# Performance work log

Measured on AMD Instinct MI355X. Metric: run time of the kernel, lower is better.

The kernel has to match this reference:

```python
import jax, jax.numpy as jnp
import numpy as np

# ---- static config (mirrors build() with the chosen init_kwargs) ----
B, H, W, C = 16, 56, 56, 128
KH, KW = 3, 3          # filter_size
SH, SW = 1, 1          # stride
NF = 256               # n_filters
IN_FEAT = C * KH * KW  # 1152
NNZ = int(1 * 0.2 * IN_FEAT * NF)  # multiple * density * n_parameters = 58982


def _make_indices():
    """Replicates the full='output' sparsity-pattern construction from build()."""
    rng = np.random.default_rng(0)
    per_col = NNZ // NF
    remain = NNZ % NF
    remain_cols = set(rng.choice(NF, remain, replace=False).tolist())
    chunks = []
    for col in rng.permutation(NF):
        k = per_col + (1 if int(col) in remain_cols else 0)
        rows = rng.choice(IN_FEAT, k, replace=False)
        chunks.append(np.stack([rows, np.full(k, col, dtype=np.int64)], axis=1))
    return np.concatenate(chunks, axis=0).astype(np.int32)  # (NNZ, 2) [row, col]


def setup_inputs() -> dict:
    key = jax.random.key(0)
    k1, k2 = jax.random.split(key)
    x = jax.random.normal(k1, (B, H, W, C), dtype=jnp.float32)
    limit = float(np.sqrt(6.0 / (IN_FEAT + NF)))  # glorot_uniform on the sparse values
    kernel = jax.random.uniform(k2, (NNZ,), jnp.float32, -limit, limit)
    bias = jnp.zeros((NF,), jnp.float32)
    indices = jnp.asarray(_make_indices())
    return {"x": x, "kernel": kernel, "bias": bias, "indices": indices}


def _im2col_valid(x):
    # tf.image.extract_patches ordering: patch positions row-major (di, dj),
    # channels fastest -> concatenate C-channel slices in (di, dj) order.
    oh = (H - KH) // SH + 1
    ow = (W - KW) // SW + 1
    cols = [x[:, di:di + oh * SH:SH, dj:dj + ow * SW:SW, :]
            for di in range(KH) for dj in range(KW)]
    return jnp.concatenate(cols, axis=-1), oh, ow  # (B, oh, ow, IN_FEAT)


def reference(x, kernel, bias, indices):
    patches, oh, ow = _im2col_valid(x)
    pm = patches.reshape(-1, IN_FEAT)  # (B*oh*ow, IN_FEAT)
    # Sparse (IN_FEAT, NF) weight: scatter values into a dense matrix
    # (indices are unique by construction, so .add == .set and is grad-safe).
    Wm = jnp.zeros((IN_FEAT, NF), dtype=pm.dtype).at[indices[:, 0], indices[:, 1]].add(kernel)
    out = pm @ Wm + bias            # sparse-dense matmul + bias
    out = jax.nn.relu(out)          # activation
    return out.reshape(B, oh, ow, NF)
```

## Files before the change

### kernel.cpp

```cpp
#include <hip/hip_runtime.h>

typedef unsigned short u16;
typedef __bf16 bf16x8 __attribute__((ext_vector_type(8)));
typedef float f32x16 __attribute__((ext_vector_type(16)));

#define B_   16
#define H_   56
#define W_   56
#define C_   128
#define OH_  54
#define OW_  54
#define NF_  256
#define KF_  1152
#define M_   46656
#define NNZ_ 58982

#define XB_ELEMS (B_*H_*W_*C_)
#define WT_ELEMS (36*4*256*8)

__device__ __forceinline__ u16 f2bf(float f) {
    unsigned u = __float_as_uint(f);
    u += 0x7FFFu + ((u >> 16) & 1u);
    return (u16)(u >> 16);
}

__device__ __forceinline__ void gload16(const void* g, void* l) {
    __builtin_amdgcn_global_load_lds(
        (const __attribute__((address_space(1))) unsigned int*)g,
        (__attribute__((address_space(3))) unsigned int*)l,
        16, 0, 0);
}

__global__ __launch_bounds__(256) void cvt_x_kernel(const float* __restrict__ x,
                                                    u16* __restrict__ xb,
                                                    u16* __restrict__ wt) {
    if (blockIdx.x < 144) {
        uint4 z = {0u, 0u, 0u, 0u};
        ((uint4*)wt)[blockIdx.x * 256 + threadIdx.x] = z;
    }
    int i = (blockIdx.x * 256 + threadIdx.x) * 8;
    float4 v0 = *(const float4*)(x + i);
    float4 v1 = *(const float4*)(x + i + 4);
    union { u16 u[8]; uint4 v; } r;
    r.u[0] = f2bf(v0.x); r.u[1] = f2bf(v0.y); r.u[2] = f2bf(v0.z); r.u[3] = f2bf(v0.w);
    r.u[4] = f2bf(v1.x); r.u[5] = f2bf(v1.y); r.u[6] = f2bf(v1.z); r.u[7] = f2bf(v1.w);
    *(uint4*)(xb + i) = r.v;
}

__global__ __launch_bounds__(256) void scatter_kernel(const float* __restrict__ kv,
                                                      const int* __restrict__ idx,
                                                      u16* __restrict__ wt) {
    int t = blockIdx.x * 256 + threadIdx.x;
    if (t >= NNZ_) return;
    int k   = idx[2*t];
    int col = idx[2*t + 1];
    int kt = k >> 5, ks = (k >> 3) & 3, e = k & 7;
    wt[(kt * 4 + ks) * 2048 + col * 8 + e] = f2bf(kv[t]);
}

__global__ __launch_bounds__(128, 2) void spconv_gemm(const u16* __restrict__ xb,
                                                      const u16* __restrict__ wt,
                                                      const float* __restrict__ bias,
                                                      float* __restrict__ out) {
    __shared__ __align__(16) u16 As[2][64 * 32];

    const int t   = threadIdx.x;
    const int l   = t & 63;
    const int w   = t >> 6;
    const int l31 = l & 31;
    const int hi  = l >> 5;

    const int nwg = gridDim.x;
    const int q = nwg >> 3, r = nwg & 7;
    const int xcd = blockIdx.x & 7, inner = blockIdx.x >> 3;
    const int wg = (xcd < r ? xcd * (q + 1) : r * (q + 1) + (xcd - r) * q) + inner;
    const int m0 = wg * 64;

    const int row0 = t >> 2;
    const int kco  = ((t & 3) ^ ((t >> 2) & 3)) * 8;
    const u16* a_base0;
    const u16* a_base1;
    {
#define MKBASE(dst, mg) do {                                   \
        int bb_  = (mg) / (OH_ * OW_);                         \
        int rem_ = (mg) % (OH_ * OW_);                         \
        int ii_  = rem_ / OW_;                                 \
        int jj_  = rem_ % OW_;                                 \
        dst = xb + ((bb_ * H_ + ii_) * W_ + jj_) * C_;         \
    } while (0)
        MKBASE(a_base0, m0 + row0);
        MKBASE(a_base1, m0 + row0 + 32);
#undef MKBASE
    }

    const char* wtb = (const char*)wt;
    const char* b0 = wtb + hi * 4096 + w * 2048 + l31 * 16;
    const char* b1 = b0 + 8192;

    int aoffr[2][2];
#pragma unroll
    for (int rb = 0; rb < 2; ++rb)
#pragma unroll
        for (int kp = 0; kp < 2; ++kp)
            aoffr[rb][kp] = ((rb * 32 + l31) * 4 + ((kp * 2 + hi) ^ (l & 3))) * 8;

    f32x16 acc[2][4];
#pragma unroll
    for (int i = 0; i < 2; ++i)
#pragma unroll
        for (int j = 0; j < 4; ++j) acc[i][j] = (f32x16)0.f;

    bf16x8 bS0[8], bS1[8];

#define LOADB(dst, base, imm) \
    asm volatile("global_load_dwordx4 %0, %1, off offset:" imm \
                 : "=v"(dst) : "v"(base) : "memory")

#define ISSUE_A(kn, bi) do {                                                \
    int g_  = (kn) >> 2;                                                    \
    int di_ = (g_ * 11) >> 5;                                               \
    int dj_ = g_ - 3 * di_;                                                 \
    int aoff_ = (di_ * W_ + dj_) * C_ + ((kn) & 3) * 32 + kco;              \
    gload16(a_base0 + aoff_, &As[bi][t * 8]);                               \
    gload16(a_base1 + aoff_, &As[bi][(t + 128) * 8]);                       \
} while (0)

#define ISSUE_B(bset) do {                                                  \
    LOADB(bset[0], b0, "0");    LOADB(bset[1], b0, "512");                  \
    LOADB(bset[2], b0, "1024"); LOADB(bset[3], b0, "1536");                 \
    LOADB(bset[4], b1, "0");    LOADB(bset[5], b1, "512");                  \
    LOADB(bset[6], b1, "1024"); LOADB(bset[7], b1, "1536");                 \
    b0 += 16384; b1 += 16384;                                               \
} while (0)

#define COMPUTE(bi, bset) do {                                              \
    bf16x8 af_[2][2];                                                       \
    _Pragma("unroll")                                                       \
    for (int rb = 0; rb < 2; ++rb)                                          \
        _Pragma("unroll")                                                   \
        for (int kp = 0; kp < 2; ++kp)                                      \
            af_[rb][kp] = *(const bf16x8*)(&As[bi][aoffr[rb][kp]]);         \
    _Pragma("unroll")                                                       \
    for (int kp = 0; kp < 2; ++kp)                                          \
        _Pragma("unroll")                                                   \
        for (int rb = 0; rb < 2; ++rb)                                      \
            _Pragma("unroll")                                               \
            for (int cb = 0; cb < 4; ++cb)                                  \
                acc[rb][cb] = __builtin_amdgcn_mfma_f32_32x32x16_bf16(      \
                    af_[rb][kp], bset[kp * 4 + cb], acc[rb][cb], 0, 0, 0);  \
} while (0)

#define WAITVM(n) asm volatile("s_waitcnt vmcnt(" #n ")" ::: "memory")
#define WAITLG0() asm volatile("s_waitcnt lgkmcnt(0)" ::: "memory")
#define SB0()     __builtin_amdgcn_sched_barrier(0)
#define BAR() do { __builtin_amdgcn_s_barrier();                            \
                   asm volatile("" ::: "memory"); } while (0)

    ISSUE_A(0, 0); ISSUE_B(bS0);
    ISSUE_A(1, 1); ISSUE_B(bS1);

    for (int k2 = 0; k2 < 17; ++k2) {
        int kn0 = 2 * k2 + 2, kn1 = 2 * k2 + 3;
        WAITVM(10); SB0(); BAR();
        COMPUTE(0, bS0);
        WAITLG0(); BAR();
        ISSUE_A(kn0, 0); ISSUE_B(bS0);
        WAITVM(10); SB0(); BAR();
        COMPUTE(1, bS1);
        WAITLG0(); BAR();
        ISSUE_A(kn1, 1); ISSUE_B(bS1);
    }
    WAITVM(10); SB0(); BAR(); COMPUTE(0, bS0);
    WAITVM(0);  SB0(); BAR(); COMPUTE(1, bS1);

#undef LOADB
#undef ISSUE_A
#undef ISSUE_B
#undef COMPUTE
#undef WAITVM
#undef WAITLG0
#undef SB0
#undef BAR

#pragma unroll
    for (int cb = 0; cb < 4; ++cb) {
        int col  = w * 128 + cb * 32 + l31;
        float bv = bias[col];
#pragma unroll
        for (int rb = 0; rb < 2; ++rb) {
#pragma unroll
            for (int rg = 0; rg < 16; ++rg) {
                int row = m0 + rb * 32 + (rg & 3) + 8 * (rg >> 2) + 4 * hi;
                out[row * NF_ + col] = fmaxf(acc[rb][cb][rg] + bv, 0.f);
            }
        }
    }
}

extern "C" void kernel_launch(void* const* d_in, const int* in_sizes, int n_in,
                              void* d_out, int out_size, void* d_ws, size_t ws_size,
                              hipStream_t stream) {
    const float* x    = (const float*)d_in[0];
    const float* kv   = (const float*)d_in[1];
    const float* bias = (const float*)d_in[2];
    const int*   idx  = (const int*)d_in[3];
    float* out = (float*)d_out;

    u16* xb  = (u16*)d_ws;
    u16* wtp = (u16*)((char*)d_ws + (size_t)XB_ELEMS * 2);

    cvt_x_kernel<<<XB_ELEMS / (256 * 8), 256, 0, stream>>>(x, xb, wtp);
    scatter_kernel<<<(NNZ_ + 255) / 256, 256, 0, stream>>>(kv, idx, wtp);
    spconv_gemm<<<M_ / 64, 128, 0, stream>>>(xb, wtp, bias, out);
}
```

Measured before the change: 45.66 us.

## Split GEMM tile across eight waves with smaller per-wave sub-tiles

The 64x256 output tile per workgroup is now computed by 8 waves (2 row groups x 4 column groups) instead of 2, so each wave holds a 32x64 accumulator and loads a quarter of the B fragments. Only half the threads issue the A-tile loads into LDS, the wait counts are adjusted per thread group, and the LDS swizzle is changed to spread bank accesses. The aim is higher occupancy and more latency hiding through lower per-wave register pressure. In exchange, each wave does less MFMA work per LDS/global load and every workgroup hits more barriers.

```diff
diff --git a/kernel.cpp b/kernel.cpp
--- a/kernel.cpp
+++ b/kernel.cpp
@@ -58,7 +58,7 @@
     wt[(kt * 4 + ks) * 2048 + col * 8 + e] = f2bf(kv[t]);
 }
 
-__global__ __launch_bounds__(128, 2) void spconv_gemm(const u16* __restrict__ xb,
+__global__ __launch_bounds__(512, 4) void spconv_gemm(const u16* __restrict__ xb,
                                                       const u16* __restrict__ wt,
                                                       const float* __restrict__ bias,
                                                       float* __restrict__ out) {
@@ -69,6 +69,8 @@
     const int w   = t >> 6;
     const int l31 = l & 31;
     const int hi  = l >> 5;
+    const int wr  = w >> 2;
+    const int wc  = w & 3;
 
     const int nwg = gridDim.x;
     const int q = nwg >> 3, r = nwg & 7;
@@ -76,102 +78,84 @@
     const int wg = (xcd < r ? xcd * (q + 1) : r * (q + 1) + (xcd - r) * q) + inner;
     const int m0 = wg * 64;
 
-    const int row0 = t >> 2;
-    const int kco  = ((t & 3) ^ ((t >> 2) & 3)) * 8;
-    const u16* a_base0;
-    const u16* a_base1;
+    const int arow = (t & 255) >> 2;
+    const int kco  = (((t & 3) ^ (arow & 3) ^ ((arow >> 2) & 3))) * 8;
+    const u16* a_base;
     {
-#define MKBASE(dst, mg) do {                                   \
-        int bb_  = (mg) / (OH_ * OW_);                         \
-        int rem_ = (mg) % (OH_ * OW_);                         \
-        int ii_  = rem_ / OW_;                                 \
-        int jj_  = rem_ % OW_;                                 \
-        dst = xb + ((bb_ * H_ + ii_) * W_ + jj_) * C_;         \
-    } while (0)
-        MKBASE(a_base0, m0 + row0);
-        MKBASE(a_base1, m0 + row0 + 32);
-#undef MKBASE
+        int mg  = m0 + arow;
+        int bb  = mg / (OH_ * OW_);
+        int rem = mg % (OH_ * OW_);
+        int ii  = rem / OW_;
+        int jj  = rem % OW_;
+        a_base = xb + ((bb * H_ + ii) * W_ + jj) * C_;
     }
 
+    const int fr = (l31 & 3) ^ ((l31 >> 2) & 3);
+    int aoff0 = (wr * 32 + l31) * 32 + ((0 * 2 + hi) ^ fr) * 8;
+    int aoff1 = (wr * 32 + l31) * 32 + ((1 * 2 + hi) ^ fr) * 8;
+
     const char* wtb = (const char*)wt;
-    const char* b0 = wtb + hi * 4096 + w * 2048 + l31 * 16;
+    const char* b0 = wtb + hi * 4096 + (wc * 64 + l31) * 16;
     const char* b1 = b0 + 8192;
 
-    int aoffr[2][2];
-#pragma unroll
-    for (int rb = 0; rb < 2; ++rb)
-#pragma unroll
-        for (int kp = 0; kp < 2; ++kp)
-            aoffr[rb][kp] = ((rb * 32 + l31) * 4 + ((kp * 2 + hi) ^ (l & 3))) * 8;
+    f32x16 acc[2];
+    acc[0] = (f32x16)0.f; acc[1] = (f32x16)0.f;
 
-    f32x16 acc[2][4];
-#pragma unroll
-    for (int i = 0; i < 2; ++i)
-#pragma unroll
-        for (int j = 0; j < 4; ++j) acc[i][j] = (f32x16)0.f;
-
-    bf16x8 bS0[8], bS1[8];
+    bf16x8 bS0[4], bS1[4];
 
 #define LOADB(dst, base, imm) \
     asm volatile("global_load_dwordx4 %0, %1, off offset:" imm \
                  : "=v"(dst) : "v"(base) : "memory")
 
 #define ISSUE_A(kn, bi) do {                                                \
-    int g_  = (kn) >> 2;                                                    \
-    int di_ = (g_ * 11) >> 5;                                               \
-    int dj_ = g_ - 3 * di_;                                                 \
-    int aoff_ = (di_ * W_ + dj_) * C_ + ((kn) & 3) * 32 + kco;              \
-    gload16(a_base0 + aoff_, &As[bi][t * 8]);                               \
-    gload16(a_base1 + aoff_, &As[bi][(t + 128) * 8]);                       \
+    if (t < 256) {                                                          \
+        int g_  = (kn) >> 2;                                                \
+        int di_ = (g_ * 11) >> 5;                                           \
+        int dj_ = g_ - 3 * di_;                                             \
+        int aoff_ = (di_ * W_ + dj_) * C_ + ((kn) & 3) * 32 + kco;          \
+        gload16(a_base + aoff_, &As[bi][t * 8]);                            \
+    }                                                                       \
 } while (0)
 
 #define ISSUE_B(bset) do {                                                  \
-    LOADB(bset[0], b0, "0");    LOADB(bset[1], b0, "512");                  \
-    LOADB(bset[2], b0, "1024"); LOADB(bset[3], b0, "1536");                 \
-    LOADB(bset[4], b1, "0");    LOADB(bset[5], b1, "512");                  \
-    LOADB(bset[6], b1, "1024"); LOADB(bset[7], b1, "1536");                 \
+    LOADB(bset[0], b0, "0");   LOADB(bset[1], b0, "512");                   \
+    LOADB(bset[2], b1, "0");   LOADB(bset[3], b1, "512");                   \
     b0 += 16384; b1 += 16384;                                               \
 } while (0)
 
 #define COMPUTE(bi, bset) do {                                              \
-    bf16x8 af_[2][2];                                                       \
-    _Pragma("unroll")                                                       \
-    for (int rb = 0; rb < 2; ++rb)                                          \
-        _Pragma("unroll")                                                   \
-        for (int kp = 0; kp < 2; ++kp)                                      \
-            af_[rb][kp] = *(const bf16x8*)(&As[bi][aoffr[rb][kp]]);         \
-    _Pragma("unroll")                                                       \
-    for (int kp = 0; kp < 2; ++kp)                                          \
-        _Pragma("unroll")                                                   \
-        for (int rb = 0; rb < 2; ++rb)                                      \
-            _Pragma("unroll")                                               \
-            for (int cb = 0; cb < 4; ++cb)                                  \
-                acc[rb][cb] = __builtin_amdgcn_mfma_f32_32x32x16_bf16(      \
-                    af_[rb][kp], bset[kp * 4 + cb], acc[rb][cb], 0, 0, 0);  \
+    bf16x8 af0_ = *(const bf16x8*)(&As[bi][aoff0]);                         \
+    acc[0] = __builtin_amdgcn_mfma_f32_32x32x16_bf16(af0_, bset[0], acc[0], 0, 0, 0); \
+    acc[1] = __builtin_amdgcn_mfma_f32_32x32x16_bf16(af0_, bset[1], acc[1], 0, 0, 0); \
+    bf16x8 af1_ = *(const bf16x8*)(&As[bi][aoff1]);                         \
+    acc[0] = __builtin_amdgcn_mfma_f32_32x32x16_bf16(af1_, bset[2], acc[0], 0, 0, 0); \
+    acc[1] = __builtin_amdgcn_mfma_f32_32x32x16_bf16(af1_, bset[3], acc[1], 0, 0, 0); \
 } while (0)
 
-#define WAITVM(n) asm volatile("s_waitcnt vmcnt(" #n ")" ::: "memory")
+#define WAITVM(nb, na) do {                                                 \
+    if (t < 256) { asm volatile("s_waitcnt vmcnt(" #nb ")" ::: "memory"); } \
+    else         { asm volatile("s_waitcnt vmcnt(" #na ")" ::: "memory"); } \
+} while (0)
 #define WAITLG0() asm volatile("s_waitcnt lgkmcnt(0)" ::: "memory")
-#define SB0()     __builtin_amdgcn_sched_barrier(0)
 #define BAR() do { __builtin_amdgcn_s_barrier();                            \
                    asm volatile("" ::: "memory"); } while (0)
 
     ISSUE_A(0, 0); ISSUE_B(bS0);
     ISSUE_A(1, 1); ISSUE_B(bS1);
 
+#pragma unroll
     for (int k2 = 0; k2 < 17; ++k2) {
-        int kn0 = 2 * k2 + 2, kn1 = 2 * k2 + 3;
-        WAITVM(10); SB0(); BAR();
+        WAITVM(5, 4); BAR();
         COMPUTE(0, bS0);
         WAITLG0(); BAR();
-        ISSUE_A(kn0, 0); ISSUE_B(bS0);
-        WAITVM(10); SB0(); BAR();
+        ISSUE_A(2 * k2 + 2, 0); ISSUE_B(bS0);
+        WAITVM(5, 4); BAR();
         COMPUTE(1, bS1);
         WAITLG0(); BAR();
-        ISSUE_A(kn1, 1); ISSUE_B(bS1);
+        ISSUE_A(2 * k2 + 3, 1); ISSUE_B(bS1);
     }
-    WAITVM(10); SB0(); BAR(); COMPUTE(0, bS0);
-    WAITVM(0);  SB0(); BAR(); COMPUTE(1, bS1);
+    WAITVM(5, 4); BAR(); COMPUTE(0, bS0);
+    WAITVM(0, 0); BAR(); COMPUTE(1, bS1);
 
 #undef LOADB
 #undef ISSUE_A
@@ -179,20 +163,16 @@
 #undef COMPUTE
 #undef WAITVM
 #undef WAITLG0
-#undef SB0
 #undef BAR
 
 #pragma unroll
-    for (int cb = 0; cb < 4; ++cb) {
-        int col  = w * 128 + cb * 32 + l31;
+    for (int cb = 0; cb < 2; ++cb) {
+        int col  = wc * 64 + cb * 32 + l31;
         float bv = bias[col];
 #pragma unroll
-        for (int rb = 0; rb < 2; ++rb) {
-#pragma unroll
-            for (int rg = 0; rg < 16; ++rg) {
-                int row = m0 + rb * 32 + (rg & 3) + 8 * (rg >> 2) + 4 * hi;
-                out[row * NF_ + col] = fmaxf(acc[rb][cb][rg] + bv, 0.f);
-            }
+        for (int rg = 0; rg < 16; ++rg) {
+            int row = m0 + wr * 32 + (rg & 3) + 8 * (rg >> 2) + 4 * hi;
+            out[row * NF_ + col] = fmaxf(acc[cb][rg] + bv, 0.f);
         }
     }
 }
@@ -211,5 +191,5 @@
 
     cvt_x_kernel<<<XB_ELEMS / (256 * 8), 256, 0, stream>>>(x, xb, wtp);
     scatter_kernel<<<(NNZ_ + 255) / 256, 256, 0, stream>>>(kv, idx, wtp);
-    spconv_gemm<<<M_ / 64, 128, 0, stream>>>(xb, wtp, bias, out);
+    spconv_gemm<<<M_ / 64, 512, 0, stream>>>(xb, wtp, bias, out);
 }
```

Result: slower. 57.77 us (+26.5%).
